# Optimization experiments

Measured on AMD Instinct MI355X. Metric: run time of the kernel, lower is better.

The kernel has to match this reference:

```python
import jax, jax.numpy as jnp
import numpy as np
from jax import lax

EPS = 1e-5
UPSAMPLE = (256, 256)


def _axis_coords(n_in, n_out, dtype):
    # PyTorch bilinear, align_corners=False: src = (i+0.5)*scale - 0.5, clamped to [0, n_in-1]
    scale = n_in / n_out
    c = jnp.clip((jnp.arange(n_out, dtype=dtype) + 0.5) * scale - 0.5, 0.0, n_in - 1)
    i0 = jnp.floor(c).astype(jnp.int32)
    i1 = jnp.minimum(i0 + 1, n_in - 1)
    w = c - i0.astype(dtype)
    return i0, i1, w


def bilinear_resize(x, out_hw):
    # x: [B, C, H, W] -> [B, C, out_h, out_w]
    B, C, H, W = x.shape
    out_h, out_w = out_hw
    y0, y1, wy = _axis_coords(H, out_h, x.dtype)
    x0, x1, wx = _axis_coords(W, out_w, x.dtype)
    wy = wy[None, None, :, None]
    ry = x[:, :, y0, :] * (1 - wy) + x[:, :, y1, :] * wy  # [B,C,out_h,W]
    out = ry[:, :, :, x0] * (1 - wx) + ry[:, :, :, x1] * wx
    return out


def reference(satellite_feature, drone_feature, gamma, beta):
    b, c, h, w = satellite_feature.shape
    # per-sample cross-correlation via grouped conv: weight [B, C, hk, wk], groups=B
    mm = lax.conv_general_dilated(
        satellite_feature.reshape(1, b * c, h, w),
        drone_feature,
        window_strides=(1, 1),
        padding='VALID',
        feature_group_count=b,
        dimension_numbers=('NCHW', 'OIHW', 'NCHW'),
    )  # [1, B, Ho, Wo]
    mm = jnp.transpose(mm, (1, 0, 2, 3))  # [B, 1, Ho, Wo]
    # BatchNorm2d(1), training mode: batch stats over (B, H, W), biased variance
    mean = jnp.mean(mm, axis=(0, 2, 3), keepdims=True)
    var = jnp.mean((mm - mean) ** 2, axis=(0, 2, 3), keepdims=True)
    mm = (mm - mean) * lax.rsqrt(var + EPS)
    mm = mm * gamma.reshape(1, -1, 1, 1) + beta.reshape(1, -1, 1, 1)
    return bilinear_resize(mm, UPSAMPLE)


def setup_inputs() -> dict:
    key = jax.random.key(0)
    k1, k2 = jax.random.split(key)
    return {
        'satellite_feature': jax.random.normal(k1, (16, 256, 64, 64), dtype=jnp.float32),
        'drone_feature': jax.random.normal(k2, (16, 256, 16, 16), dtype=jnp.float32),
        'gamma': jnp.ones((1,), dtype=jnp.float32),
        'beta': jnp.zeros((1,), dtype=jnp.float32),
    }
```

## Files before the change

kernel.cpp:

```cpp
#include <hip/hip_runtime.h>

using f32x4  = __attribute__((ext_vector_type(4))) float;
using bf16x8 = __attribute__((ext_vector_type(8))) short;

__device__ __forceinline__ unsigned short f2bf(float f) {
    union { float f; unsigned int u; } v; v.f = f;
    unsigned int r = v.u + 0x7fffu + ((v.u >> 16) & 1u);
    return (unsigned short)(r >> 16);
}

__device__ __forceinline__ float bf2f(unsigned short u) {
    union { unsigned int u; float f; } v; v.u = ((unsigned int)u) << 16;
    return v.f;
}

__global__ __launch_bounds__(256) void transposeD(
    const float* __restrict__ x, unsigned short* __restrict__ y) {
    __shared__ float tile[32][33];
    int b  = blockIdx.z;
    int p0 = blockIdx.x * 32;
    int c0 = blockIdx.y * 32;
    const float* xb = x + (size_t)b * 256 * 256;
    unsigned short* yb = y + (size_t)b * 256 * 256;
    int tx = threadIdx.x, ty = threadIdx.y;
    #pragma unroll
    for (int i = 0; i < 32; i += 8)
        tile[ty + i][tx] = xb[(size_t)(c0 + ty + i) * 256 + (p0 + tx)];
    __syncthreads();
    int tid = ty * 32 + tx;
    #pragma unroll
    for (int k = 0; k < 2; ++k) {
        int wi = tid * 2 + k;
        int pl = wi >> 4;
        int cp = wi & 15;
        unsigned short lo = f2bf(tile[2 * cp][pl]);
        unsigned short hi = f2bf(tile[2 * cp + 1][pl]);
        unsigned int packed = (unsigned int)lo | ((unsigned int)hi << 16);
        *reinterpret_cast<unsigned int*>(&yb[(size_t)(p0 + pl) * 256 + (c0 + 2 * cp)]) = packed;
    }
}

__global__ __launch_bounds__(256, 4) void conv_fused(
    const float* __restrict__ S,
    const unsigned short* __restrict__ Dt,
    float* __restrict__ P) {
    __shared__ __align__(16) char lds[64 * 262 * 2];
    char* base = lds;

    int b = blockIdx.x >> 6;
    int r = blockIdx.x & 63;
    int tid = threadIdx.x;

    {
        int sub = tid & 3;
        int cl  = tid >> 2;
        f32x4 v[16];
        #pragma unroll
        for (int chunk = 0; chunk < 4; ++chunk) {
            int c = chunk * 64 + cl;
            const float* src = S + (((size_t)(b * 256 + c) * 64 + r) * 64);
            #pragma unroll
            for (int k = 0; k < 4; ++k)
                v[chunk * 4 + k] = *reinterpret_cast<const f32x4*>(src + 16 * k + 4 * sub);
        }
        #pragma unroll
        for (int chunk = 0; chunk < 4; ++chunk) {
            int c = chunk * 64 + cl;
            #pragma unroll
            for (int k = 0; k < 4; ++k) {
                int p = 16 * k + 4 * sub;
                #pragma unroll
                for (int e = 0; e < 4; ++e) {
                    int pe = p + e;
                    int off = pe * 512 + ((((c >> 3) ^ (pe & 15))) << 4) + ((c & 7) << 1);
                    *reinterpret_cast<unsigned short*>(base + off) = f2bf(v[chunk * 4 + k][e]);
                }
            }
        }
    }
    __syncthreads();

    int w    = tid >> 6;
    int lane = tid & 63;
    int m    = lane & 15;
    int kg   = lane >> 4;

    const unsigned short* Db = Dt + ((size_t)(b * 256 + 64 * w)) * 256;

    f32x4 acc[4][4];
    #pragma unroll
    for (int i = 0; i < 4; ++i)
        #pragma unroll
        for (int j = 0; j < 4; ++j)
            acc[i][j] = f32x4{0.f, 0.f, 0.f, 0.f};

    #pragma unroll
    for (int step = 0; step < 8; ++step) {
        bf16x8 bfr[4];
        #pragma unroll
        for (int n = 0; n < 4; ++n)
            bfr[n] = *reinterpret_cast<const bf16x8*>(Db + (size_t)(16 * n + m) * 256 + step * 32 + kg * 8);
        bf16x8 af[4];
        #pragma unroll
        for (int pa = 0; pa < 4; ++pa) {
            int p = 16 * pa + m;
            int slot = (4 * step + kg) ^ m;
            af[pa] = *reinterpret_cast<const bf16x8*>(base + p * 512 + slot * 16);
        }
        #pragma unroll
        for (int pa = 0; pa < 4; ++pa)
            #pragma unroll
            for (int n = 0; n < 4; ++n)
                acc[pa][n] = __builtin_amdgcn_mfma_f32_16x16x32_bf16(af[pa], bfr[n], acc[pa][n], 0, 0, 0);
    }

    __syncthreads();

    unsigned short* gt = (unsigned short*)base;
    #pragma unroll
    for (int pa = 0; pa < 4; ++pa)
        #pragma unroll
        for (int n = 0; n < 4; ++n)
            #pragma unroll
            for (int t = 0; t < 4; ++t) {
                int row = 16 * pa + 4 * kg + t;
                int col = 64 * w + 16 * n + m;
                gt[row * 262 + col] = f2bf(acc[pa][n][t]);
            }
    __syncthreads();

    int ilo = (r > 48) ? (r - 48) : 0;
    int ihi = (r < 15) ? r : 15;
    int total = (ihi - ilo + 1) * 49;
    for (int o = tid; o < total; o += 256) {
        int i = ilo + o / 49;
        int x = o % 49;
        float s = 0.f;
        int qb = 16 * i;
        #pragma unroll
        for (int j = 0; j < 16; ++j)
            s += bf2f(gt[(x + j) * 262 + qb + j]);
        P[((size_t)((b * 64 + r) * 16 + i)) * 52 + x] = s;
    }
}

__global__ __launch_bounds__(256) void reduce_kernel(
    const float* __restrict__ P, float* __restrict__ mm) {
    int idx = blockIdx.x * 256 + threadIdx.x;
    if (idx >= 38416) return;
    int b  = idx / 2401;
    int yx = idx % 2401;
    int y  = yx / 49;
    int x  = yx % 49;
    float s = 0.f;
    #pragma unroll
    for (int i = 0; i < 16; ++i)
        s += P[((size_t)((b * 64 + y + i) * 16 + i)) * 52 + x];
    mm[idx] = s;
}

__global__ __launch_bounds__(256) void conv_naive(
    const float* __restrict__ S, const float* __restrict__ D, float* __restrict__ mm) {
    int blk = blockIdx.x;
    int b = blk / 2401;
    int yx = blk % 2401;
    int y = yx / 49, x = yx % 49;
    int c = threadIdx.x;
    const float* Sp = S + (((size_t)b * 256 + c) * 64 + y) * 64 + x;
    const float* Dp = D + ((size_t)b * 256 + c) * 256;
    float s = 0.f;
    #pragma unroll
    for (int i = 0; i < 16; ++i)
        #pragma unroll 4
        for (int j = 0; j < 16; ++j)
            s += Sp[i * 64 + j] * Dp[i * 16 + j];
    __shared__ float red[256];
    red[c] = s;
    __syncthreads();
    for (int st = 128; st > 0; st >>= 1) {
        if (c < st) red[c] += red[c + st];
        __syncthreads();
    }
    if (c == 0) mm[blk] = red[0];
}

__global__ __launch_bounds__(1024) void stats_kernel(
    const float* __restrict__ mm, float* __restrict__ stats) {
    __shared__ float ssum[1024];
    __shared__ float ssq[1024];
    int tid = threadIdx.x;
    float s = 0.f, q = 0.f;
    for (int i = tid; i < 38416; i += 1024) {
        float v = mm[i];
        s += v; q += v * v;
    }
    ssum[tid] = s; ssq[tid] = q;
    __syncthreads();
    for (int st = 512; st > 0; st >>= 1) {
        if (tid < st) { ssum[tid] += ssum[tid + st]; ssq[tid] += ssq[tid + st]; }
        __syncthreads();
    }
    if (tid == 0) {
        float mean = ssum[0] / 38416.f;
        float var  = ssq[0] / 38416.f - mean * mean;
        stats[0] = mean;
        stats[1] = rsqrtf(var + 1e-5f);
    }
}

__global__ __launch_bounds__(256) void bilinear_kernel(
    const float* __restrict__ mm, const float* __restrict__ stats,
    const float* __restrict__ gamma, const float* __restrict__ beta,
    float* __restrict__ out) {
    int idx = blockIdx.x * 256 + threadIdx.x;
    int b  = idx >> 16;
    int oy = (idx >> 8) & 255;
    int ox = idx & 255;
    const float scale = 49.0f / 256.0f;
    float cy = fminf(fmaxf((oy + 0.5f) * scale - 0.5f, 0.0f), 48.0f);
    int y0 = (int)cy; int y1 = min(y0 + 1, 48); float wy = cy - (float)y0;
    float cx = fminf(fmaxf((ox + 0.5f) * scale - 0.5f, 0.0f), 48.0f);
    int x0 = (int)cx; int x1 = min(x0 + 1, 48); float wx = cx - (float)x0;
    const float* mb = mm + (size_t)b * 2401;
    float v00 = mb[y0 * 49 + x0];
    float v01 = mb[y0 * 49 + x1];
    float v10 = mb[y1 * 49 + x0];
    float v11 = mb[y1 * 49 + x1];
    float r0 = v00 * (1.f - wy) + v10 * wy;
    float r1 = v01 * (1.f - wy) + v11 * wy;
    float v  = r0 * (1.f - wx) + r1 * wx;
    float mean = stats[0], rstd = stats[1];
    v = (v - mean) * rstd * gamma[0] + beta[0];
    out[idx] = v;
}

extern "C" void kernel_launch(void* const* d_in, const int* in_sizes, int n_in,
                              void* d_out, int out_size, void* d_ws, size_t ws_size,
                              hipStream_t stream) {
    const float* S     = (const float*)d_in[0];
    const float* D     = (const float*)d_in[1];
    const float* gamma = (const float*)d_in[2];
    const float* beta  = (const float*)d_in[3];
    float* out = (float*)d_out;

    char* ws = (char*)d_ws;
    const size_t sizeDt = (size_t)16 * 256 * 256 * 2;
    const size_t sizeMm = (size_t)38416 * 4;
    const size_t sizeP  = (size_t)16 * 64 * 16 * 52 * 4;
    const size_t offDt = 0;
    const size_t offMm = offDt + sizeDt;
    const size_t offStats = offMm + sizeMm;
    const size_t offP = (offStats + 2 * sizeof(float) + 255) & ~(size_t)255;
    const size_t needFast = offP + sizeP;

    bool fast = (ws_size >= needFast);
    float* mm;
    float* stats;
    if (fast) {
        mm    = (float*)(ws + offMm);
        stats = (float*)(ws + offStats);
    } else {
        mm    = (float*)ws;
        stats = (float*)(ws + sizeMm);
    }

    if (fast) {
        unsigned short* Dt = (unsigned short*)(ws + offDt);
        float* P = (float*)(ws + offP);
        transposeD<<<dim3(8, 8, 16), dim3(32, 8), 0, stream>>>(D, Dt);
        conv_fused<<<1024, 256, 0, stream>>>(S, Dt, P);
        reduce_kernel<<<151, 256, 0, stream>>>(P, mm);
    } else {
        conv_naive<<<16 * 2401, 256, 0, stream>>>(S, D, mm);
    }
    stats_kernel<<<1, 1024, 0, stream>>>(mm, stats);
    bilinear_kernel<<<4096, 256, 0, stream>>>(mm, stats, gamma, beta, out);
}
```

Measured before the change: 52.12 us.

## Fuse batch-norm stats into reduce kernel and prefetch conv operands

Removes the single-block stats kernel: the reduce kernel now does a block-level reduction of sum and sum of squares and atomically adds them into stats, which transposeD zeroes first. The bilinear kernel derives mean and rstd from the raw sums. Separately, conv_fused's satellite staging is rewritten to use vectorized ushort4 LDS writes with a new swizzle, and D fragments are register double-buffered across k-steps. This adds float atomics (order-dependent results) and more register pressure.

```diff
diff --git a/kernel.cpp b/kernel.cpp
--- a/kernel.cpp
+++ b/kernel.cpp
@@ -15,7 +15,7 @@
 }
 
 __global__ __launch_bounds__(256) void transposeD(
-    const float* __restrict__ x, unsigned short* __restrict__ y) {
+    const float* __restrict__ x, unsigned short* __restrict__ y, float* __restrict__ stats) {
     __shared__ float tile[32][33];
     int b  = blockIdx.z;
     int p0 = blockIdx.x * 32;
@@ -38,6 +38,10 @@
         unsigned int packed = (unsigned int)lo | ((unsigned int)hi << 16);
         *reinterpret_cast<unsigned int*>(&yb[(size_t)(p0 + pl) * 256 + (c0 + 2 * cp)]) = packed;
     }
+    if (blockIdx.x == 0 && blockIdx.y == 0 && blockIdx.z == 0 && tid == 0) {
+        stats[0] = 0.f;
+        stats[1] = 0.f;
+    }
 }
 
 __global__ __launch_bounds__(256, 4) void conv_fused(
@@ -51,41 +55,48 @@
     int r = blockIdx.x & 63;
     int tid = threadIdx.x;
 
-    {
-        int sub = tid & 3;
-        int cl  = tid >> 2;
-        f32x4 v[16];
-        #pragma unroll
-        for (int chunk = 0; chunk < 4; ++chunk) {
-            int c = chunk * 64 + cl;
-            const float* src = S + (((size_t)(b * 256 + c) * 64 + r) * 64);
-            #pragma unroll
-            for (int k = 0; k < 4; ++k)
-                v[chunk * 4 + k] = *reinterpret_cast<const f32x4*>(src + 16 * k + 4 * sub);
-        }
-        #pragma unroll
-        for (int chunk = 0; chunk < 4; ++chunk) {
-            int c = chunk * 64 + cl;
-            #pragma unroll
-            for (int k = 0; k < 4; ++k) {
-                int p = 16 * k + 4 * sub;
-                #pragma unroll
-                for (int e = 0; e < 4; ++e) {
-                    int pe = p + e;
-                    int off = pe * 512 + ((((c >> 3) ^ (pe & 15))) << 4) + ((c & 7) << 1);
-                    *reinterpret_cast<unsigned short*>(base + off) = f2bf(v[chunk * 4 + k][e]);
-                }
-            }
-        }
-    }
-    __syncthreads();
-
     int w    = tid >> 6;
     int lane = tid & 63;
     int m    = lane & 15;
     int kg   = lane >> 4;
-
     const unsigned short* Db = Dt + ((size_t)(b * 256 + 64 * w)) * 256;
+
+    int px = tid & 15;
+    int cq = tid >> 4;
+    const float* Sbr = S + ((size_t)b * 256 * 64 + r) * 64;
+
+    f32x4 v[4][4];
+    #pragma unroll
+    for (int rho = 0; rho < 4; ++rho) {
+        int c0 = rho * 64 + 4 * cq;
+        #pragma unroll
+        for (int j = 0; j < 4; ++j)
+            v[rho][j] = *reinterpret_cast<const f32x4*>(Sbr + (size_t)(c0 + j) * 4096 + 4 * px);
+    }
+    bf16x8 bcur[4];
+    #pragma unroll
+    for (int n = 0; n < 4; ++n)
+        bcur[n] = *reinterpret_cast<const bf16x8*>(Db + (size_t)(16 * n + m) * 256 + kg * 8);
+    __builtin_amdgcn_sched_barrier(0);
+
+    #pragma unroll
+    for (int rho = 0; rho < 4; ++rho) {
+        int slot = 8 * rho + (cq >> 1);
+        int half = cq & 1;
+        #pragma unroll
+        for (int e = 0; e < 4; ++e) {
+            int p = 4 * px + e;
+            int swz = (p & 15) ^ (p >> 4);
+            ushort4 o;
+            o.x = f2bf(v[rho][0][e]);
+            o.y = f2bf(v[rho][1][e]);
+            o.z = f2bf(v[rho][2][e]);
+            o.w = f2bf(v[rho][3][e]);
+            *reinterpret_cast<ushort4*>(base + p * 512 + ((slot ^ swz) << 4) + half * 8) = o;
+        }
+    }
+    asm volatile("s_waitcnt lgkmcnt(0)" ::: "memory");
+    __builtin_amdgcn_s_barrier();
 
     f32x4 acc[4][4];
     #pragma unroll
@@ -96,22 +107,28 @@
 
     #pragma unroll
     for (int step = 0; step < 8; ++step) {
-        bf16x8 bfr[4];
-        #pragma unroll
-        for (int n = 0; n < 4; ++n)
-            bfr[n] = *reinterpret_cast<const bf16x8*>(Db + (size_t)(16 * n + m) * 256 + step * 32 + kg * 8);
+        bf16x8 bnext[4];
+        if (step < 7) {
+            #pragma unroll
+            for (int n = 0; n < 4; ++n)
+                bnext[n] = *reinterpret_cast<const bf16x8*>(
+                    Db + (size_t)(16 * n + m) * 256 + (step + 1) * 32 + kg * 8);
+        }
         bf16x8 af[4];
         #pragma unroll
         for (int pa = 0; pa < 4; ++pa) {
             int p = 16 * pa + m;
-            int slot = (4 * step + kg) ^ m;
-            af[pa] = *reinterpret_cast<const bf16x8*>(base + p * 512 + slot * 16);
+            int slot = (4 * step + kg) ^ m ^ pa;
+            af[pa] = *reinterpret_cast<const bf16x8*>(base + p * 512 + (slot << 4));
         }
         #pragma unroll
         for (int pa = 0; pa < 4; ++pa)
             #pragma unroll
             for (int n = 0; n < 4; ++n)
-                acc[pa][n] = __builtin_amdgcn_mfma_f32_16x16x32_bf16(af[pa], bfr[n], acc[pa][n], 0, 0, 0);
+                acc[pa][n] = __builtin_amdgcn_mfma_f32_16x16x32_bf16(af[pa], bcur[n], acc[pa][n], 0, 0, 0);
+        #pragma unroll
+        for (int n = 0; n < 4; ++n)
+            bcur[n] = bnext[n];
     }
 
     __syncthreads();
@@ -145,18 +162,33 @@
 }
 
 __global__ __launch_bounds__(256) void reduce_kernel(
-    const float* __restrict__ P, float* __restrict__ mm) {
+    const float* __restrict__ P, float* __restrict__ mm, float* __restrict__ stats) {
     int idx = blockIdx.x * 256 + threadIdx.x;
-    if (idx >= 38416) return;
-    int b  = idx / 2401;
-    int yx = idx % 2401;
-    int y  = yx / 49;
-    int x  = yx % 49;
     float s = 0.f;
-    #pragma unroll
-    for (int i = 0; i < 16; ++i)
-        s += P[((size_t)((b * 64 + y + i) * 16 + i)) * 52 + x];
-    mm[idx] = s;
+    if (idx < 38416) {
+        int b  = idx / 2401;
+        int yx = idx % 2401;
+        int y  = yx / 49;
+        int x  = yx % 49;
+        #pragma unroll
+        for (int i = 0; i < 16; ++i)
+            s += P[((size_t)((b * 64 + y + i) * 16 + i)) * 52 + x];
+        mm[idx] = s;
+    }
+    __shared__ float rs[256];
+    __shared__ float rq[256];
+    int tid = threadIdx.x;
+    rs[tid] = (idx < 38416) ? s : 0.f;
+    rq[tid] = (idx < 38416) ? s * s : 0.f;
+    __syncthreads();
+    for (int st = 128; st > 0; st >>= 1) {
+        if (tid < st) { rs[tid] += rs[tid + st]; rq[tid] += rq[tid + st]; }
+        __syncthreads();
+    }
+    if (tid == 0) {
+        atomicAdd(&stats[0], rs[0]);
+        atomicAdd(&stats[1], rq[0]);
+    }
 }
 
 __global__ __launch_bounds__(256) void conv_naive(
@@ -201,10 +233,8 @@
         __syncthreads();
     }
     if (tid == 0) {
-        float mean = ssum[0] / 38416.f;
-        float var  = ssq[0] / 38416.f - mean * mean;
-        stats[0] = mean;
-        stats[1] = rsqrtf(var + 1e-5f);
+        stats[0] = ssum[0];
+        stats[1] = ssq[0];
     }
 }
 
@@ -229,7 +259,10 @@
     float r0 = v00 * (1.f - wy) + v10 * wy;
     float r1 = v01 * (1.f - wy) + v11 * wy;
     float v  = r0 * (1.f - wx) + r1 * wx;
-    float mean = stats[0], rstd = stats[1];
+    const float invN = 1.0f / 38416.0f;
+    float mean = stats[0] * invN;
+    float var  = stats[1] * invN - mean * mean;
+    float rstd = rsqrtf(var + 1e-5f);
     v = (v - mean) * rstd * gamma[0] + beta[0];
     out[idx] = v;
 }
@@ -267,12 +300,12 @@
     if (fast) {
         unsigned short* Dt = (unsigned short*)(ws + offDt);
         float* P = (float*)(ws + offP);
-        transposeD<<<dim3(8, 8, 16), dim3(32, 8), 0, stream>>>(D, Dt);
+        transposeD<<<dim3(8, 8, 16), dim3(32, 8), 0, stream>>>(D, Dt, stats);
         conv_fused<<<1024, 256, 0, stream>>>(S, Dt, P);
-        reduce_kernel<<<151, 256, 0, stream>>>(P, mm);
+        reduce_kernel<<<151, 256, 0, stream>>>(P, mm, stats);
     } else {
         conv_naive<<<16 * 2401, 256, 0, stream>>>(S, D, mm);
-    }
-    stats_kernel<<<1, 1024, 0, stream>>>(mm, stats);
+        stats_kernel<<<1, 1024, 0, stream>>>(mm, stats);
+    }
     bilinear_kernel<<<4096, 256, 0, stream>>>(mm, stats, gamma, beta, out);
 }
```

Measured after the change: 43.14 us. 1.21x faster.
